# Performance work log

Measured on AMD Instinct MI355X. Metric: run time of the kernel, lower is better.

## Reference

```python
import jax, jax.numpy as jnp
from jax import lax
import numpy as np

B, N, S, K, C = 8, 16384, 1024, 32, 256


def setup_inputs() -> dict:
    key = jax.random.key(0)
    ks = jax.random.split(key, 8)
    def lin(k, o, i):
        return (jax.random.normal(k, (o, i), jnp.float32) / np.sqrt(i)).astype(jnp.float32)
    return {
        "x": jax.random.normal(ks[0], (B, N, 3), jnp.float32),
        "Wqkv": lin(ks[1], 3 * C, 3), "bqkv": jnp.zeros((3 * C,), jnp.float32),
        "g1": lin(ks[2], C, C), "bg1": jnp.zeros((C,), jnp.float32),
        "g2": lin(ks[3], C, C), "bg2": jnp.zeros((C,), jnp.float32),
        "Wo": lin(ks[4], C, C), "bo": jnp.zeros((C,), jnp.float32),
        "p1": lin(ks[5], 128, 3), "bp1": jnp.zeros((128,), jnp.float32),
        "p2": lin(ks[6], C, 128), "bp2": jnp.zeros((C,), jnp.float32),
    }


def _fps(xyz, num_patches):
    # furthest point sampling, deterministic start at index 0 (matches pointnet2 CUDA op)
    b, n, _ = xyz.shape
    def body(carry, _):
        dmin, far = carry
        c = jnp.take_along_axis(xyz, far[:, None, None], axis=1)[:, 0]  # [B,3]
        d = jnp.sum((xyz - c[:, None, :]) ** 2, axis=-1)                # [B,N]
        dmin = jnp.minimum(dmin, d)
        return (dmin, jnp.argmax(dmin, axis=-1)), far
    init = (jnp.full((b, n), 1e10, xyz.dtype), jnp.zeros((b,), jnp.int32))
    _, idx = lax.scan(body, init, None, length=num_patches)
    return jnp.transpose(idx)  # [B,S]


def _gelu(x):
    return jax.nn.gelu(x, approximate=False)  # torch nn.GELU default = exact erf


def reference(x, Wqkv, bqkv, g1, bg1, g2, bg2, Wo, bo, p1, bp1, p2, bp2):
    scale = C ** (-0.5)
    fps_idx = _fps(x, S)                                        # [B,S]
    centroid = jnp.take_along_axis(x, fps_idx[..., None], axis=1)  # [B,S,3]
    # square_distance(centroid, x): [B,S,N]
    d = (jnp.sum(centroid ** 2, -1)[..., None]
         + jnp.sum(x ** 2, -1)[:, None, :]
         - 2.0 * jnp.einsum('bsc,bnc->bsn', centroid, x))
    _, knn = lax.top_k(-d, K)                                   # [B,S,K] smallest-k (== argsort[:, :, :k])
    grouped = jax.vmap(lambda pts, i: pts[i])(x, knn)           # [B,S,K,3]
    # 1x1 Conv2d over channel dim == linear on last axis
    qkv = grouped @ Wqkv.T + bqkv                               # [B,S,K,3C]
    q, k_, v = jnp.split(qkv, 3, axis=-1)
    q = q.max(axis=2); k_ = k_.max(axis=2); v = v.max(axis=2)   # [B,S,C]
    h = _gelu((q - k_) @ g1.T + bg1) @ g2.T + bg2               # fc_gamma MLP
    attn = jax.nn.softmax(h * scale, axis=-1)                   # softmax over channels
    pos = _gelu(centroid @ p1.T + bp1) @ p2.T + bp2             # [B,S,C]
    return (attn * v) @ Wo.T + bo + pos                         # [B,S,C]
```

## Files before the change

### kernel.cpp

```cpp
#include <hip/hip_runtime.h>
#include <hip/hip_bf16.h>
#include <cstdint>

#define B_ 8
#define N_ 16384
#define S_ 1024
#define K_ 32
#define C_ 256
#define RR 8

__device__ __forceinline__ float gelu_f(float x){
  return 0.5f * x * (1.0f + erff(x * 0.70710678118654752f));
}

__device__ __forceinline__ float dist2_f(float px, float py, float pz,
                                         float cx, float cy, float cz){
  float dx = px - cx, dy = py - cy, dz = pz - cz;
  return dx*dx + dy*dy + dz*dz;
}

__global__ void prep_kernel(const float* __restrict__ x,
                            const float* __restrict__ g1,
                            const float* __restrict__ g2,
                            const float* __restrict__ Wo,
                            const float* __restrict__ p2,
                            float* __restrict__ xT,
                            float* __restrict__ g1T,
                            float* __restrict__ g2T,
                            float* __restrict__ WoT,
                            float* __restrict__ p2T,
                            float4* __restrict__ xP){
  int u = blockIdx.x * 256 + threadIdx.x;
  if (u < B_*N_){
    int b = u >> 14, n = u & (N_-1);
    const float* p = x + (size_t)u * 3;
    float X = p[0], Y = p[1], Z = p[2];
    xT[((size_t)b*3+0)*N_ + n] = X;
    xT[((size_t)b*3+1)*N_ + n] = Y;
    xT[((size_t)b*3+2)*N_ + n] = Z;
    xP[u] = make_float4(X, Y, Z, 0.0f);
  } else if (u < B_*N_ + 65536){
    int v = u - B_*N_; int i = v >> 8, j = v & 255;
    g1T[v] = g1[j*256 + i];
  } else if (u < B_*N_ + 2*65536){
    int v = u - B_*N_ - 65536; int i = v >> 8, j = v & 255;
    g2T[v] = g2[j*256 + i];
  } else if (u < B_*N_ + 3*65536){
    int v = u - B_*N_ - 2*65536; int i = v >> 8, j = v & 255;
    WoT[v] = Wo[j*256 + i];
  } else if (u < B_*N_ + 3*65536 + 32768){
    int v = u - B_*N_ - 3*65536; int i = v >> 8, j = v & 255;
    p2T[v] = p2[j*128 + i];
  }
}

__global__ __launch_bounds__(1024, 1) void fps_kernel(const float4* __restrict__ xP,
                                                      float* __restrict__ cent){
  int b = blockIdx.x;
  int tid = threadIdx.x;
  const float4* P = xP + (size_t)b * N_;
  __shared__ float xs[N_];
  __shared__ float ys[N_];
  __shared__ float wmax[16];
  __shared__ int islot[2];
  __shared__ float centb[S_*3];
  float pz[16], dm[16];
  #pragma unroll
  for (int i=0;i<16;i++){
    float4 p = P[i*1024 + tid];
    xs[i*1024 + tid] = p.x;
    ys[i*1024 + tid] = p.y;
    pz[i] = p.z;
    dm[i] = 1e10f;
  }
  #pragma unroll
  for (int i=0;i<16;i++) asm volatile("" : "+v"(pz[i]));
  if (tid < 2) islot[tid] = 0x7FFFFFFF;
  __syncthreads();
  float4 c4 = P[0];
  for (int s=0; s<S_; s++){
    int cur = s & 1;
    if (tid == 0){
      centb[s*3+0]=c4.x; centb[s*3+1]=c4.y; centb[s*3+2]=c4.z;
    }
    float cx=c4.x, cy=c4.y, cz=c4.z;
    float m = 0.0f;
    #pragma unroll
    for (int i=0;i<16;i++){
      float dx = xs[i*1024 + tid] - cx;
      float dy = ys[i*1024 + tid] - cy;
      float dz = pz[i] - cz;
      float d = fmaf(dz, dz, fmaf(dy, dy, dx*dx));
      float dmn = fminf(dm[i], d);
      dm[i] = dmn;
      m = fmaxf(m, dmn);
    }
    float wm = m;
    #pragma unroll
    for (int off=32; off; off>>=1) wm = fmaxf(wm, __shfl_xor(wm, off));
    if ((tid & 63) == 0) wmax[tid>>6] = wm;
    __syncthreads();
    if (tid == 0) islot[cur^1] = 0x7FFFFFFF;
    float g01 = fmaxf(fmaxf(wmax[0],wmax[1]),  fmaxf(wmax[2],wmax[3]));
    float g23 = fmaxf(fmaxf(wmax[4],wmax[5]),  fmaxf(wmax[6],wmax[7]));
    float g45 = fmaxf(fmaxf(wmax[8],wmax[9]),  fmaxf(wmax[10],wmax[11]));
    float g67 = fmaxf(fmaxf(wmax[12],wmax[13]),fmaxf(wmax[14],wmax[15]));
    float gm = fmaxf(fmaxf(g01,g23), fmaxf(g45,g67));
    if (wm == gm){
      int cidx = 0x7FFFFFFF;
      #pragma unroll
      for (int i=15;i>=0;i--){ if (dm[i]==gm) cidx = i*1024 + tid; }
      if (cidx != 0x7FFFFFFF) atomicMin(&islot[cur], cidx);
    }
    __syncthreads();
    int far = islot[cur];
    c4 = P[far];
  }
  __syncthreads();
  for (int i = tid; i < S_*3; i += 1024) cent[(size_t)b*S_*3 + i] = centb[i];
}

__global__ __launch_bounds__(256) void knn_qkv_kernel(const float* __restrict__ xT,
                                                      const float* __restrict__ cent,
                                                      const float* __restrict__ Wqkv,
                                                      const float* __restrict__ bqkv,
                                                      float* __restrict__ qkv){
  __shared__ unsigned hist[RR][256];
  __shared__ unsigned candB[RR][256];
  __shared__ int      candI[RR][256];
  __shared__ int      selI[RR][32];
  __shared__ float    pts[RR][32][3];
  __shared__ int      cnt[RR];
  __shared__ int      Bstar[RR];
  int tid = threadIdx.x;
  int row0 = blockIdx.x * RR;
  int b = row0 >> 10;
  const float* X = xT + (size_t)b*3*N_;
  const float* Y = X + N_;
  const float* Z = Y + N_;
  float cx[RR], cy[RR], cz[RR];
  #pragma unroll
  for (int r=0;r<RR;r++){
    const float* c = cent + ((size_t)row0 + r)*3;
    cx[r]=c[0]; cy[r]=c[1]; cz[r]=c[2];
  }
  for (int i=tid; i<RR*256; i+=256) ((unsigned*)hist)[i] = 0u;
  if (tid < RR) cnt[tid]=0;
  __syncthreads();
  for (int i=0;i<64;i++){
    int g = i*256 + tid;
    float px=X[g], py=Y[g], pz=Z[g];
    #pragma unroll
    for (int r=0;r<RR;r++){
      float d = dist2_f(px,py,pz,cx[r],cy[r],cz[r]);
      int key = (int)(__float_as_uint(d) >> 20) - 840;
      key = min(max(key,0),255);
      atomicAdd(&hist[r][key], 1u);
    }
  }
  __syncthreads();
  int w = tid >> 6, lane = tid & 63;
  for (int half=0; half<2; half++){
    int r = half*4 + w;
    uint4 h4 = ((uint4*)&hist[r][0])[lane];
    unsigned cum = h4.x + h4.y + h4.z + h4.w;
    for (int off=1; off<64; off<<=1){
      unsigned t = __shfl_up(cum, off);
      if (lane >= off) cum += t;
    }
    unsigned long long mask = __ballot(cum >= 32u);
    int lb = __ffsll((unsigned long long)mask) - 1;
    unsigned cumPrev = __shfl(cum, lb>0 ? lb-1 : 0);
    if (lane == lb){
      unsigned c0 = (lb==0) ? 0u : cumPrev;
      unsigned hh[4] = {h4.x,h4.y,h4.z,h4.w};
      int bs = lb*4 + 3;
      for (int k=0;k<4;k++){
        if (c0 + hh[k] >= 32u){ bs = lb*4 + k; break; }
        c0 += hh[k];
      }
      Bstar[r] = bs;
    }
  }
  __syncthreads();
  int bsr[RR];
  #pragma unroll
  for (int r=0;r<RR;r++) bsr[r] = min(Bstar[r]+1, 255);
  for (int i=0;i<64;i++){
    int g = i*256 + tid;
    float px=X[g], py=Y[g], pz=Z[g];
    #pragma unroll
    for (int r=0;r<RR;r++){
      float d = dist2_f(px,py,pz,cx[r],cy[r],cz[r]);
      unsigned bits = __float_as_uint(d);
      int key = min(max((int)(bits>>20) - 840, 0), 255);
      if (key <= bsr[r]){
        int pos = atomicAdd(&cnt[r], 1);
        if (pos < 256){ candB[r][pos] = bits; candI[r][pos] = g; }
      }
    }
  }
  __syncthreads();
  for (int half=0; half<2; half++){
    int r = half*4 + w;
    int L = min(cnt[r], 256);
    for (int j=lane; j<L; j+=64){
      unsigned mb = candB[r][j]; int mi = candI[r][j];
      int rank = 0;
      for (int t=0;t<L;t++){
        unsigned tb = candB[r][t]; int ti = candI[r][t];
        rank += (tb < mb || (tb == mb && ti < mi)) ? 1 : 0;
      }
      if (rank < 32) selI[r][rank] = mi;
    }
  }
  __syncthreads();
  { int r = tid >> 5, p = tid & 31;
    int g = selI[r][p];
    pts[r][p][0]=X[g]; pts[r][p][1]=Y[g]; pts[r][p][2]=Z[g]; }
  __syncthreads();
  float w0[3], w1[3], w2[3], bb[3];
  #pragma unroll
  for (int c3=0;c3<3;c3++){
    int c = tid + c3*256;
    w0[c3]=Wqkv[c*3+0]; w1[c3]=Wqkv[c*3+1]; w2[c3]=Wqkv[c*3+2]; bb[c3]=bqkv[c];
  }
  for (int r=0;r<RR;r++){
    float m0=-1e30f, m1=-1e30f, m2=-1e30f;
    #pragma unroll
    for (int p=0;p<32;p++){
      float px=pts[r][p][0], py=pts[r][p][1], pz=pts[r][p][2];
      m0 = fmaxf(m0, w0[0]*px + w1[0]*py + w2[0]*pz);
      m1 = fmaxf(m1, w0[1]*px + w1[1]*py + w2[1]*pz);
      m2 = fmaxf(m2, w0[2]*px + w1[2]*py + w2[2]*pz);
    }
    float* o = qkv + ((size_t)row0 + r)*768;
    o[tid      ] = m0 + bb[0];
    o[tid + 256] = m1 + bb[1];
    o[tid + 512] = m2 + bb[2];
  }
}

template<int KD>
__device__ __forceinline__ void gemm_tile(const float* A_, const float* __restrict__ Wt,
                                          int rb, int lane, float acc[4][4]){
  const float4* W4 = (const float4*)Wt;
  for (int i0=0; i0<(KD>>2); i0++){
    float4 wv0 = W4[(i0*4+0)*64 + lane];
    float4 wv1 = W4[(i0*4+1)*64 + lane];
    float4 wv2 = W4[(i0*4+2)*64 + lane];
    float4 wv3 = W4[(i0*4+3)*64 + lane];
    #pragma unroll
    for (int r=0;r<4;r++){
      float4 a = ((const float4*)(A_ + (size_t)(rb+r)*KD))[i0];
      acc[r][0] = fmaf(a.x,wv0.x,fmaf(a.y,wv1.x,fmaf(a.z,wv2.x,fmaf(a.w,wv3.x,acc[r][0]))));
      acc[r][1] = fmaf(a.x,wv0.y,fmaf(a.y,wv1.y,fmaf(a.z,wv2.y,fmaf(a.w,wv3.y,acc[r][1]))));
      acc[r][2] = fmaf(a.x,wv0.z,fmaf(a.y,wv1.z,fmaf(a.z,wv2.z,fmaf(a.w,wv3.z,acc[r][2]))));
      acc[r][3] = fmaf(a.x,wv0.w,fmaf(a.y,wv1.w,fmaf(a.z,wv2.w,fmaf(a.w,wv3.w,acc[r][3]))));
    }
  }
}

__global__ __launch_bounds__(512, 2) void stage2_kernel(const float* __restrict__ qkv,
                                                        const float* __restrict__ cent,
                                                        const float* __restrict__ g1T,
                                                        const float* __restrict__ bg1,
                                                        const float* __restrict__ g2T,
                                                        const float* __restrict__ bg2,
                                                        const float* __restrict__ WoT,
                                                        const float* __restrict__ bo,
                                                        const float* __restrict__ p1,
                                                        const float* __restrict__ bp1,
                                                        const float* __restrict__ p2T,
                                                        const float* __restrict__ bp2,
                                                        float* __restrict__ out){
  __shared__ float A[32][256];
  __shared__ float T[32][128];
  __shared__ float CC[32][3];
  int tid = threadIdx.x;
  int w = tid >> 6, lane = tid & 63;
  int rb = w * 4;
  int row0 = blockIdx.x * 32;
  const float4* qkv4 = (const float4*)qkv;
  #pragma unroll
  for (int t=0;t<4;t++){
    int fi = t*512 + tid;
    int r = fi >> 6, c4 = fi & 63;
    float4 q = qkv4[(size_t)(row0+r)*192 + c4];
    float4 k = qkv4[(size_t)(row0+r)*192 + 64 + c4];
    ((float4*)&A[r][0])[c4] = make_float4(q.x-k.x, q.y-k.y, q.z-k.z, q.w-k.w);
  }
  if (tid < 96) ((float*)CC)[tid] = cent[(size_t)row0*3 + tid];
  __syncthreads();
  #pragma unroll
  for (int t=0;t<8;t++){
    int e = t*512 + tid;
    int r = e >> 7, c = e & 127;
    float tv = CC[r][0]*p1[c*3+0] + CC[r][1]*p1[c*3+1] + CC[r][2]*p1[c*3+2] + bp1[c];
    T[r][c] = gelu_f(tv);
  }
  __syncthreads();
  float acc[4][4];
  #pragma unroll
  for (int r=0;r<4;r++){ acc[r][0]=0.f; acc[r][1]=0.f; acc[r][2]=0.f; acc[r][3]=0.f; }
  gemm_tile<256>(&A[0][0], g1T, rb, lane, acc);
  {
    float4 bg = ((const float4*)bg1)[lane];
    #pragma unroll
    for (int r=0;r<4;r++){
      float4 g;
      g.x = gelu_f(acc[r][0] + bg.x);
      g.y = gelu_f(acc[r][1] + bg.y);
      g.z = gelu_f(acc[r][2] + bg.z);
      g.w = gelu_f(acc[r][3] + bg.w);
      ((float4*)&A[rb+r][0])[lane] = g;
    }
  }
  #pragma unroll
  for (int r=0;r<4;r++){ acc[r][0]=0.f; acc[r][1]=0.f; acc[r][2]=0.f; acc[r][3]=0.f; }
  gemm_tile<256>(&A[0][0], g2T, rb, lane, acc);
  {
    float4 bg = ((const float4*)bg2)[lane];
    const float scale = 0.0625f;
    #pragma unroll
    for (int r=0;r<4;r++){
      float h0 = acc[r][0]+bg.x, h1 = acc[r][1]+bg.y, h2 = acc[r][2]+bg.z, h3 = acc[r][3]+bg.w;
      float mx = fmaxf(fmaxf(h0,h1), fmaxf(h2,h3));
      for (int off=1; off<64; off<<=1) mx = fmaxf(mx, __shfl_xor(mx, off));
      float e0 = __expf((h0-mx)*scale), e1 = __expf((h1-mx)*scale);
      float e2 = __expf((h2-mx)*scale), e3 = __expf((h3-mx)*scale);
      float sm = e0+e1+e2+e3;
      for (int off=1; off<64; off<<=1) sm += __shfl_xor(sm, off);
      float inv = 1.0f / sm;
      float4 v4 = qkv4[(size_t)(row0+rb+r)*192 + 128 + lane];
      ((float4*)&A[rb+r][0])[lane] =
          make_float4(e0*inv*v4.x, e1*inv*v4.y, e2*inv*v4.z, e3*inv*v4.w);
    }
  }
  #pragma unroll
  for (int r=0;r<4;r++){ acc[r][0]=0.f; acc[r][1]=0.f; acc[r][2]=0.f; acc[r][3]=0.f; }
  gemm_tile<256>(&A[0][0], WoT, rb, lane, acc);
  gemm_tile<128>(&T[0][0], p2T, rb, lane, acc);
  {
    float4 bov = ((const float4*)bo)[lane];
    float4 bpv = ((const float4*)bp2)[lane];
    #pragma unroll
    for (int r=0;r<4;r++){
      float4 o;
      o.x = acc[r][0] + bov.x + bpv.x;
      o.y = acc[r][1] + bov.y + bpv.y;
      o.z = acc[r][2] + bov.z + bpv.z;
      o.w = acc[r][3] + bov.w + bpv.w;
      ((float4*)out)[(size_t)(row0+rb+r)*64 + lane] = o;
    }
  }
}

extern "C" void kernel_launch(void* const* d_in, const int* in_sizes, int n_in,
                              void* d_out, int out_size, void* d_ws, size_t ws_size,
                              hipStream_t stream) {
  const float* x    = (const float*)d_in[0];
  const float* Wqkv = (const float*)d_in[1];
  const float* bqkv = (const float*)d_in[2];
  const float* g1   = (const float*)d_in[3];
  const float* bg1  = (const float*)d_in[4];
  const float* g2   = (const float*)d_in[5];
  const float* bg2  = (const float*)d_in[6];
  const float* Wo   = (const float*)d_in[7];
  const float* bo   = (const float*)d_in[8];
  const float* p1   = (const float*)d_in[9];
  const float* bp1  = (const float*)d_in[10];
  const float* p2   = (const float*)d_in[11];
  const float* bp2  = (const float*)d_in[12];
  float* out = (float*)d_out;
  float* ws = (float*)d_ws;

  float* xT   = ws;
  float* cent = xT + 393216;
  float* qkv  = cent + 24576;
  float* g1T  = qkv + 6291456;
  float* g2T  = g1T + 65536;
  float* WoT  = g2T + 65536;
  float* p2T  = WoT + 65536;
  float4* xP  = (float4*)(p2T + 32768);

  hipLaunchKernelGGL(prep_kernel, dim3(1408), dim3(256), 0, stream,
                     x, g1, g2, Wo, p2, xT, g1T, g2T, WoT, p2T, xP);
  hipLaunchKernelGGL(fps_kernel, dim3(B_), dim3(1024), 0, stream, xP, cent);
  hipLaunchKernelGGL(knn_qkv_kernel, dim3(B_*S_/RR), dim3(256), 0, stream,
                     xT, cent, Wqkv, bqkv, qkv);
  hipLaunchKernelGGL(stage2_kernel, dim3(B_*S_/32), dim3(512), 0, stream,
                     qkv, cent, g1T, bg1, g2T, bg2, WoT, bo, p1, bp1, p2T, bp2, out);
}
```

Before: 1.751 ms.

## Morton-sort points in FPS and skip wave updates via bounding-box pruning

The FPS kernel now bins each batch's points into a 12-bit Morton grid with a shared-memory counting sort, so each wave owns a spatially compact set of 1024 points. Each wave keeps its bounding box and skips the distance update whenever the box's minimum distance to the new centroid is at least the wave's current max-min distance, reusing the cached max. Ties are resolved through the sort map to keep the lowest original index. This adds setup cost and a global scratch map stored in the qkv buffer, and the savings depend on the spatial coherence of the input distribution, since the grid range is hard-coded to [-5,5].

```diff
diff --git a/kernel.cpp b/kernel.cpp
--- a/kernel.cpp
+++ b/kernel.cpp
@@ -17,6 +17,24 @@
                                          float cx, float cy, float cz){
   float dx = px - cx, dy = py - cy, dz = pz - cz;
   return dx*dx + dy*dy + dz*dz;
+}
+
+__device__ __forceinline__ unsigned mort12(float4 p){
+  unsigned ix = (unsigned)fminf(fmaxf((p.x + 5.f)*1.6f, 0.f), 15.99f);
+  unsigned iy = (unsigned)fminf(fmaxf((p.y + 5.f)*1.6f, 0.f), 15.99f);
+  unsigned iz = (unsigned)fminf(fmaxf((p.z + 5.f)*1.6f, 0.f), 15.99f);
+  unsigned m = 0;
+  #pragma unroll
+  for (int t=0;t<4;t++){
+    m |= ((ix>>t)&1u) << (3*t+2);
+    m |= ((iy>>t)&1u) << (3*t+1);
+    m |= ((iz>>t)&1u) << (3*t+0);
+  }
+  return m;
+}
+
+__device__ __forceinline__ float bcast0(float v){
+  return __int_as_float(__builtin_amdgcn_readfirstlane(__float_as_int(v)));
 }
 
 __global__ void prep_kernel(const float* __restrict__ x,
@@ -55,28 +73,77 @@
 }
 
 __global__ __launch_bounds__(1024, 1) void fps_kernel(const float4* __restrict__ xP,
-                                                      float* __restrict__ cent){
+                                                      float* __restrict__ cent,
+                                                      unsigned* __restrict__ map){
   int b = blockIdx.x;
   int tid = threadIdx.x;
+  int lane = tid & 63, wv = tid >> 6;
   const float4* P = xP + (size_t)b * N_;
-  __shared__ float xs[N_];
-  __shared__ float ys[N_];
-  __shared__ float wmax[16];
+  unsigned* bmap = map + (size_t)b * N_;
+  __shared__ __align__(16) float xys[2*N_];
+  __shared__ __align__(16) float wmax[16];
+  __shared__ unsigned wsum[16];
   __shared__ int islot[2];
   __shared__ float centb[S_*3];
-  float pz[16], dm[16];
+  unsigned* hist = (unsigned*)xys;
+
+  for (int i=tid; i<4096; i+=1024) hist[i] = 0u;
+  __syncthreads();
   #pragma unroll
   for (int i=0;i<16;i++){
     float4 p = P[i*1024 + tid];
-    xs[i*1024 + tid] = p.x;
-    ys[i*1024 + tid] = p.y;
-    pz[i] = p.z;
-    dm[i] = 1e10f;
+    atomicAdd(&hist[mort12(p)], 1u);
+  }
+  __syncthreads();
+  uint4 h4 = ((uint4*)hist)[tid];
+  unsigned s4 = h4.x+h4.y+h4.z+h4.w;
+  unsigned inc = s4;
+  for (int off=1; off<64; off<<=1){ unsigned t=__shfl_up(inc,off); if (lane>=off) inc += t; }
+  if (lane==63) wsum[wv] = inc;
+  __syncthreads();
+  if (tid==0){ unsigned run=0; for (int k=0;k<16;k++){ unsigned t=wsum[k]; wsum[k]=run; run+=t; } }
+  __syncthreads();
+  {
+    unsigned tb = wsum[wv] + (inc - s4);
+    uint4 o; o.x = tb; o.y = o.x + h4.x; o.z = o.y + h4.y; o.w = o.z + h4.z;
+    ((uint4*)hist)[tid] = o;
+  }
+  __syncthreads();
+  #pragma unroll
+  for (int i=0;i<16;i++){
+    float4 p = P[i*1024 + tid];
+    unsigned dst = atomicAdd(&hist[mort12(p)], 1u);
+    bmap[dst] = (unsigned)(i*1024 + tid);
+  }
+  __syncthreads();
+
+  int base = wv*1024 + lane;
+  float pz[16], dm[16];
+  float lx=1e30f, ly=1e30f, lz=1e30f, hx=-1e30f, hy=-1e30f, hz=-1e30f;
+  #pragma unroll
+  for (int i=0;i<16;i++){
+    int slot = base + i*64;
+    unsigned orig = bmap[slot];
+    float4 p = P[orig];
+    ((float2*)xys)[slot] = make_float2(p.x, p.y);
+    pz[i] = p.z; dm[i] = 1e10f;
+    lx=fminf(lx,p.x); hx=fmaxf(hx,p.x);
+    ly=fminf(ly,p.y); hy=fmaxf(hy,p.y);
+    lz=fminf(lz,p.z); hz=fmaxf(hz,p.z);
   }
   #pragma unroll
   for (int i=0;i<16;i++) asm volatile("" : "+v"(pz[i]));
+  #pragma unroll
+  for (int off=1; off<64; off<<=1){
+    lx=fminf(lx,__shfl_xor(lx,off)); hx=fmaxf(hx,__shfl_xor(hx,off));
+    ly=fminf(ly,__shfl_xor(ly,off)); hy=fmaxf(hy,__shfl_xor(hy,off));
+    lz=fminf(lz,__shfl_xor(lz,off)); hz=fmaxf(hz,__shfl_xor(hz,off));
+  }
+  lx=bcast0(lx); hx=bcast0(hx); ly=bcast0(ly); hy=bcast0(hy); lz=bcast0(lz); hz=bcast0(hz);
+  if (lane==0) wmax[wv] = 1e10f;
   if (tid < 2) islot[tid] = 0x7FFFFFFF;
   __syncthreads();
+
   float4 c4 = P[0];
   for (int s=0; s<S_; s++){
     int cur = s & 1;
@@ -84,33 +151,48 @@
       centb[s*3+0]=c4.x; centb[s*3+1]=c4.y; centb[s*3+2]=c4.z;
     }
     float cx=c4.x, cy=c4.y, cz=c4.z;
-    float m = 0.0f;
-    #pragma unroll
-    for (int i=0;i<16;i++){
-      float dx = xs[i*1024 + tid] - cx;
-      float dy = ys[i*1024 + tid] - cy;
-      float dz = pz[i] - cz;
-      float d = fmaf(dz, dz, fmaf(dy, dy, dx*dx));
-      float dmn = fminf(dm[i], d);
-      dm[i] = dmn;
-      m = fmaxf(m, dmn);
-    }
-    float wm = m;
-    #pragma unroll
-    for (int off=32; off; off>>=1) wm = fmaxf(wm, __shfl_xor(wm, off));
-    if ((tid & 63) == 0) wmax[tid>>6] = wm;
+    float tx = fmaxf(fmaxf(lx-cx, cx-hx), 0.f);
+    float ty = fmaxf(fmaxf(ly-cy, cy-hy), 0.f);
+    float tz = fmaxf(fmaxf(lz-cz, cz-hz), 0.f);
+    float md2 = fmaf(tz,tz, fmaf(ty,ty, tx*tx));
+    float wcap = wmax[wv];
+    float wm;
+    if (md2 * 0.9999f < wcap){
+      float m = 0.f;
+      #pragma unroll
+      for (int i=0;i<16;i++){
+        float2 xy = ((const float2*)xys)[base + i*64];
+        float dx = xy.x - cx, dy = xy.y - cy, dz = pz[i] - cz;
+        float d = fmaf(dz, dz, fmaf(dy, dy, dx*dx));
+        float dmn = fminf(dm[i], d);
+        dm[i] = dmn;
+        m = fmaxf(m, dmn);
+      }
+      wm = m;
+      #pragma unroll
+      for (int off=32; off; off>>=1) wm = fmaxf(wm, __shfl_xor(wm, off));
+      if (lane==0) wmax[wv] = wm;
+    } else {
+      wm = wcap;
+    }
     __syncthreads();
     if (tid == 0) islot[cur^1] = 0x7FFFFFFF;
-    float g01 = fmaxf(fmaxf(wmax[0],wmax[1]),  fmaxf(wmax[2],wmax[3]));
-    float g23 = fmaxf(fmaxf(wmax[4],wmax[5]),  fmaxf(wmax[6],wmax[7]));
-    float g45 = fmaxf(fmaxf(wmax[8],wmax[9]),  fmaxf(wmax[10],wmax[11]));
-    float g67 = fmaxf(fmaxf(wmax[12],wmax[13]),fmaxf(wmax[14],wmax[15]));
-    float gm = fmaxf(fmaxf(g01,g23), fmaxf(g45,g67));
+    float4 wa = ((const float4*)wmax)[0];
+    float4 wb = ((const float4*)wmax)[1];
+    float4 wc = ((const float4*)wmax)[2];
+    float4 wd = ((const float4*)wmax)[3];
+    float g0 = fmaxf(fmaxf(wa.x,wa.y), fmaxf(wa.z,wa.w));
+    float g1 = fmaxf(fmaxf(wb.x,wb.y), fmaxf(wb.z,wb.w));
+    float g2 = fmaxf(fmaxf(wc.x,wc.y), fmaxf(wc.z,wc.w));
+    float g3 = fmaxf(fmaxf(wd.x,wd.y), fmaxf(wd.z,wd.w));
+    float gm = fmaxf(fmaxf(g0,g1), fmaxf(g2,g3));
     if (wm == gm){
-      int cidx = 0x7FFFFFFF;
+      int cand = 0x7FFFFFFF;
       #pragma unroll
-      for (int i=15;i>=0;i--){ if (dm[i]==gm) cidx = i*1024 + tid; }
-      if (cidx != 0x7FFFFFFF) atomicMin(&islot[cur], cidx);
+      for (int i=0;i<16;i++){
+        if (dm[i] == gm) cand = min(cand, (int)bmap[base + i*64]);
+      }
+      if (cand != 0x7FFFFFFF) atomicMin(&islot[cur], cand);
     }
     __syncthreads();
     int far = islot[cur];
@@ -383,10 +465,11 @@
   float* WoT  = g2T + 65536;
   float* p2T  = WoT + 65536;
   float4* xP  = (float4*)(p2T + 32768);
+  unsigned* map = (unsigned*)qkv;
 
   hipLaunchKernelGGL(prep_kernel, dim3(1408), dim3(256), 0, stream,
                      x, g1, g2, Wo, p2, xT, g1T, g2T, WoT, p2T, xP);
-  hipLaunchKernelGGL(fps_kernel, dim3(B_), dim3(1024), 0, stream, xP, cent);
+  hipLaunchKernelGGL(fps_kernel, dim3(B_), dim3(1024), 0, stream, xP, cent, map);
   hipLaunchKernelGGL(knn_qkv_kernel, dim3(B_*S_/RR), dim3(256), 0, stream,
                      xT, cent, Wqkv, bqkv, qkv);
   hipLaunchKernelGGL(stage2_kernel, dim3(B_*S_/32), dim3(512), 0, stream,
```

Result: slower. 1.855 ms (+5.9%).
